# Kernel optimization log

Measured on AMD Instinct MI355X. Metric: run time of the kernel, lower is better.

## Reference

```python
import jax, jax.numpy as jnp
import numpy as np
from jax import lax

N_C = 2
T = 5
NE = 17   # equality constraints per (sample, t)
NV = 24   # variables per (sample, t): p(4), f(4), f_e(4), alpha1(2), alpha2(2), gamma(4), gamma_e(4)
ITERS = 400
B = 512

F_MASK = jnp.zeros((NV,), bool).at[4:8].set(True)     # L1-penalized coords (f)
NN_MASK = jnp.zeros((NV,), bool).at[12:24].set(True)  # nonneg coords (alpha1, alpha2, gamma, gamma_e)


def _conv(x, w, b):
    return lax.conv_general_dilated(x, w, (1, 1), 'VALID',
                                    dimension_numbers=('NCHW', 'OIHW', 'NCHW')) + b[None, :, None, None]


def _maxpool(x, k):
    return lax.reduce_window(x, -jnp.inf, lax.max, (1, 1, k, k), (1, 1, k, k), 'VALID')


def _encoder(img, cw1, cb1, cw2, cb2, w3, b3, w4, b4):
    h = jax.nn.relu(_maxpool(_conv(img, cw1, cb1), 2))   # (B,10,20,20)
    h = jax.nn.relu(_maxpool(_conv(h, cw2, cb2), 4))     # (B,20,4,4)
    h = h.reshape(h.shape[0], -1)                        # (B,320)
    h = jax.nn.relu(h @ w3.T + b3)                       # dropout is eval-mode identity
    return jax.nn.relu(h @ w4.T + b4)                    # (B,100)


def _mlp(h, w1, b1, w2, b2, w3, b3):
    h = jax.nn.relu(h @ w1.T + b1)  # dropout eval-mode identity
    h = jax.nn.relu(h @ w2.T + b2)
    return h @ w3.T + b3


def _build_Ab(r, ddr, fc, p_e, fc_e, v, p_r):
    # one (t)-slice: r(3), ddr(3), fc(8), p_e(4), fc_e(8), v(8), p_r(4) -> A(17,24), b(17)
    A = jnp.zeros((NE, NV))
    b = jnp.zeros((NE,))
    # force balance x: sum(f) + f_e0 + f_e1 = ddr0  (original f[:20] covers all 4 rows, f[20:] empty)
    A = A.at[0, 4:8].set(1.0).at[0, 8].set(1.0).at[0, 9].set(1.0)
    b = b.at[0].set(ddr[0])
    # force balance y: f_e2 + f_e3 = ddr1
    A = A.at[1, 10].set(1.0).at[1, 11].set(1.0)
    b = b.at[1].set(ddr[1])
    # torque balance
    A = A.at[2, 6].set(p_r[0] - r[0]).at[2, 4].set(-(p_r[2] - r[1]))
    A = A.at[2, 7].set(p_r[1] - r[0]).at[2, 5].set(-(p_r[3] - r[1]))
    A = A.at[2, 10].set(p_e[0] - r[0]).at[2, 8].set(-(p_e[2] - r[1]))
    A = A.at[2, 11].set(p_e[1] - r[0]).at[2, 9].set(-(p_e[3] - r[1]))
    b = b.at[2].set(ddr[2])
    for c in range(N_C):
        # p = alpha1*v_a + alpha2*v_b, alpha1+alpha2=1
        A = A.at[3 + 3 * c, c].set(1.0).at[3 + 3 * c, 12 + c].set(-v[2 * c]).at[3 + 3 * c, 14 + c].set(-v[2 * c + 2])
        A = A.at[4 + 3 * c, c + 2].set(1.0).at[4 + 3 * c, 12 + c].set(-v[2 * c + 1]).at[4 + 3 * c, 14 + c].set(-v[2 * c + 3])
        A = A.at[5 + 3 * c, 12 + c].set(1.0).at[5 + 3 * c, 14 + c].set(1.0)
        b = b.at[5 + 3 * c].set(1.0)
        # friction cone: f = gamma1*fc_a + gamma2*fc_b
        A = A.at[9 + 2 * c, 16 + c].set(fc[2 * c]).at[9 + 2 * c, 18 + c].set(fc[2 * c + 2]).at[9 + 2 * c, 4 + c].set(-1.0)
        A = A.at[10 + 2 * c, 16 + c].set(fc[2 * c + 1]).at[10 + 2 * c, 18 + c].set(fc[2 * c + 3]).at[10 + 2 * c, 6 + c].set(-1.0)
    # external force cones
    A = A.at[13, 20].set(fc_e[0]).at[13, 21].set(fc_e[2]).at[13, 8].set(-1.0)
    A = A.at[14, 20].set(fc_e[1]).at[14, 21].set(fc_e[3]).at[14, 10].set(-1.0)
    A = A.at[15, 22].set(fc_e[4]).at[15, 23].set(fc_e[6]).at[15, 9].set(-1.0)
    A = A.at[16, 22].set(fc_e[5]).at[16, 23].set(fc_e[7]).at[16, 11].set(-1.0)
    return A, b


def _specnorm(A):
    def body(i, u):
        u = A.T @ (A @ u)
        return u / (jnp.linalg.norm(u) + 1e-12)
    u = lax.fori_loop(0, 25, body, jnp.ones((A.shape[-1],), A.dtype))
    return jnp.linalg.norm(A @ u)


def _solve_lp(A, b):
    # batched: min ||f||_1  s.t.  A z = b,  z[nn] >= 0   via PDHG (Chambolle-Pock)
    P = A.shape[0]
    L = lax.stop_gradient(jax.vmap(_specnorm)(A))
    tau = (0.9 / (L + 1e-8))[:, None]
    sig = tau

    def step(carry, _):
        z, zb, y = carry
        y = y + sig * (jnp.einsum('pev,pv->pe', A, zb) - b)
        g = z - tau * jnp.einsum('pev,pe->pv', A, y)
        zn = jnp.where(F_MASK, jnp.sign(g) * jnp.maximum(jnp.abs(g) - tau, 0.0),
                       jnp.where(NN_MASK, jnp.maximum(g, 0.0), g))
        return (zn, 2.0 * zn - z, y), None

    z0 = jnp.zeros((P, NV))
    y0 = jnp.zeros((P, NE))
    (z, _, _), _ = lax.scan(step, (z0, z0, y0), None, length=ITERS)
    return z


def reference(xtraj, x, x_img, cw1, cb1, cw2, cb2, w3, b3, w4, b4,
              pw1, pb1, pw2, pb2, pw3, pb3, vw1, vb1, vw2, vb2, vw3, vb3):
    Bn = xtraj.shape[0]
    img = x_img.reshape(Bn, 1, 50, 50)
    e = _encoder(img, cw1, cb1, cw2, cb2, w3, b3, w4, b4)       # (B,100)
    h = jnp.concatenate([e, xtraj], axis=1)                     # (B,145)
    p_r = _mlp(h, pw1, pb1, pw2, pb2, pw3, pb3)                 # (B,20)
    v = _mlp(h, vw1, vb1, vw2, vb2, vw3, vb3)                   # (B,40)
    r = xtraj[:, :15].reshape(Bn, 3, T)
    ddr = xtraj[:, 30:45].reshape(Bn, 3, T)
    fc = x[:, 20:60].reshape(Bn, 8, T)
    p_e = x[:, 60:80].reshape(Bn, 4, T)
    fc_e = x[:, 80:120].reshape(Bn, 8, T)
    vM = v.reshape(Bn, 8, T)
    p_rM = p_r.reshape(Bn, 4, T)

    def flat(a):  # (B,d,T) -> (B*T, d)
        return jnp.swapaxes(a, 1, 2).reshape(Bn * T, a.shape[1])

    A, bvec = jax.vmap(_build_Ab)(flat(r), flat(ddr), flat(fc), flat(p_e), flat(fc_e), flat(vM), flat(p_rM))
    z = _solve_lp(A, bvec).reshape(Bn, T, NV)
    p = jnp.swapaxes(z[..., 0:4], 1, 2).reshape(Bn, 20)   # matches p.view(1,-1) C-order of (4,5)
    f = jnp.swapaxes(z[..., 4:8], 1, 2).reshape(Bn, 20)
    dp = p_r - x[:, 0:20]
    dv = v - x[:, 120:160]
    return 100.0 * jnp.concatenate([p, f, 10.0 * dp, 10.0 * dv], axis=1)  # (B,100)


def setup_inputs() -> dict:
    key = jax.random.key(0)
    ks = jax.random.split(key, 32)

    def rn(k, shape, s=0.05):
        return (s * jax.random.normal(k, shape)).astype(jnp.float32)

    return {
        'xtraj': rn(ks[0], (B, 45), 1.0),
        'x': rn(ks[1], (B, 160), 1.0),
        'x_img': rn(ks[2], (B, 2500), 1.0),
        'cw1': rn(ks[3], (10, 1, 11, 11)), 'cb1': rn(ks[4], (10,)),
        'cw2': rn(ks[5], (20, 10, 5, 5)), 'cb2': rn(ks[6], (20,)),
        'w3': rn(ks[7], (150, 320)), 'b3': rn(ks[8], (150,)),
        'w4': rn(ks[9], (100, 150)), 'b4': rn(ks[10], (100,)),
        'pw1': rn(ks[11], (100, 145)), 'pb1': rn(ks[12], (100,)),
        'pw2': rn(ks[13], (100, 100)), 'pb2': rn(ks[14], (100,)),
        'pw3': rn(ks[15], (20, 100)), 'pb3': rn(ks[16], (20,)),
        'vw1': rn(ks[17], (100, 145)), 'vb1': rn(ks[18], (100,)),
        'vw2': rn(ks[19], (100, 100)), 'vb2': rn(ks[20], (100,)),
        'vw3': rn(ks[21], (40, 100)), 'vb3': rn(ks[22], (40,)),
    }
```

## Files before the change

### kernel.cpp

```cpp
#include <hip/hip_runtime.h>

__global__ __launch_bounds__(128) void conv1_kernel(
    const float* __restrict__ x_img, const float* __restrict__ cw1,
    const float* __restrict__ cb1, float* __restrict__ h1)
{
    const int blk = blockIdx.x;
    const int b = blk >> 2;
    const int c = blk & 3;
    const int tid = threadIdx.x;

    __shared__ __align__(16) float s_img[1000];

    const float* img = x_img + (size_t)b * 2500 + (size_t)(10 * c) * 50;
    for (int i = tid; i < 1000; i += 128) s_img[i] = img[i];
    __syncthreads();

    if (tid < 100) {
        const int ly = tid / 20, px = tid % 20;
        const int py = 5 * c + ly;
        const int C = 2 * px;
        float acc0[10], acc1[10], acc2[10], acc3[10];
        #pragma unroll
        for (int oc = 0; oc < 10; ++oc) { acc0[oc] = 0.f; acc1[oc] = 0.f; acc2[oc] = 0.f; acc3[oc] = 0.f; }
        for (int r = 0; r < 12; ++r) {
            float v[12];
            #pragma unroll
            for (int j = 0; j < 6; ++j) {
                float2 t = *(const float2*)&s_img[(2 * ly + r) * 50 + C + 2 * j];
                v[2 * j] = t.x; v[2 * j + 1] = t.y;
            }
            if (r < 11) {
                #pragma unroll
                for (int oc = 0; oc < 10; ++oc) {
                    #pragma unroll
                    for (int kx = 0; kx < 11; ++kx) {
                        float w0 = cw1[oc * 121 + r * 11 + kx];
                        acc0[oc] = fmaf(v[kx], w0, acc0[oc]);
                        acc1[oc] = fmaf(v[kx + 1], w0, acc1[oc]);
                    }
                }
            }
            if (r >= 1) {
                #pragma unroll
                for (int oc = 0; oc < 10; ++oc) {
                    #pragma unroll
                    for (int kx = 0; kx < 11; ++kx) {
                        float w1 = cw1[oc * 121 + (r - 1) * 11 + kx];
                        acc2[oc] = fmaf(v[kx], w1, acc2[oc]);
                        acc3[oc] = fmaf(v[kx + 1], w1, acc3[oc]);
                    }
                }
            }
        }
        float* hb = h1 + (size_t)b * 4000 + py * 20 + px;
        #pragma unroll
        for (int oc = 0; oc < 10; ++oc) {
            float m = fmaxf(fmaxf(acc0[oc], acc1[oc]), fmaxf(acc2[oc], acc3[oc]));
            hb[oc * 400] = fmaxf(m + cb1[oc], 0.f);
        }
    }
}

__device__ const signed char AZ_IDX[32][8] = {
    {4,5,6,7,8,9,0,0},{10,11,0,0,0,0,0,0},{4,5,6,7,8,9,10,11},
    {0,12,14,0,0,0,0,0},{2,12,14,0,0,0,0,0},{12,14,0,0,0,0,0,0},
    {1,13,15,0,0,0,0,0},{3,13,15,0,0,0,0,0},{13,15,0,0,0,0,0,0},
    {16,18,4,0,0,0,0,0},{16,18,6,0,0,0,0,0},{17,19,5,0,0,0,0,0},
    {17,19,7,0,0,0,0,0},{20,21,8,0,0,0,0,0},{20,21,10,0,0,0,0,0},
    {22,23,9,0,0,0,0,0},{22,23,11,0,0,0,0,0},
    {0},{0},{0},{0},{0},{0},{0},{0},{0},{0},{0},{0},{0},{0},{0}
};
__device__ const signed char AZ_SEL[32][8] = {
    {1,1,1,1,1,1,0,0},{1,1,0,0,0,0,0,0},{3,4,5,6,7,8,9,10},
    {1,11,13,0,0,0,0,0},{1,12,14,0,0,0,0,0},{1,1,0,0,0,0,0,0},
    {1,13,15,0,0,0,0,0},{1,14,16,0,0,0,0,0},{1,1,0,0,0,0,0,0},
    {17,19,2,0,0,0,0,0},{18,20,2,0,0,0,0,0},{19,21,2,0,0,0,0,0},
    {20,22,2,0,0,0,0,0},{23,25,2,0,0,0,0,0},{24,26,2,0,0,0,0,0},
    {27,29,2,0,0,0,0,0},{28,30,2,0,0,0,0,0},
    {0},{0},{0},{0},{0},{0},{0},{0},{0},{0},{0},{0},{0},{0},{0}
};
__device__ const signed char AT_IDX[32][3] = {
    {3,0,0},{6,0,0},{4,0,0},{7,0,0},
    {0,2,9},{0,2,11},{0,2,10},{0,2,12},{0,2,13},{0,2,15},{1,2,14},{1,2,16},
    {3,4,5},{6,7,8},{3,4,5},{6,7,8},
    {9,10,0},{11,12,0},{9,10,0},{11,12,0},
    {13,14,0},{13,14,0},{15,16,0},{15,16,0},
    {0},{0},{0},{0},{0},{0},{0},{0}
};
__device__ const signed char WBA[32] = {0,0,0,0, 4,4,4,4, 4,4,4,4, 0,0,0,0, 4,4,4,4, 8,8,8,8, 0,0,0,0,0,0,0,0};
__device__ const signed char WBB[32] = {12,12,12,12, 8,8,8,8, 8,8,8,8, 12,12,12,12, 16,16,16,16, 20,20,20,20, 0,0,0,0,0,0,0,0};
__device__ const signed char WBC[32] = {0,0,0,0, 16,16,16,16, 20,20,20,20, 0,0,0,0, 0,0,0,0, 0,0,0,0, 0,0,0,0,0,0,0,0};

__global__ __launch_bounds__(320) void head_lp_kernel(
    const float* __restrict__ xtraj, const float* __restrict__ x,
    const float* __restrict__ h1g,
    const float* __restrict__ cw2, const float* __restrict__ cb2,
    const float* __restrict__ w3, const float* __restrict__ b3,
    const float* __restrict__ w4, const float* __restrict__ b4,
    const float* __restrict__ pw1, const float* __restrict__ pb1,
    const float* __restrict__ pw2, const float* __restrict__ pb2,
    const float* __restrict__ pw3, const float* __restrict__ pb3,
    const float* __restrict__ vw1, const float* __restrict__ vb1,
    const float* __restrict__ vw2, const float* __restrict__ vb2,
    const float* __restrict__ vw3, const float* __restrict__ vb3,
    float* __restrict__ out)
{
    const int b = blockIdx.x;
    const int tid = threadIdx.x;

    __shared__ __align__(16) float s_h1[4000];
    __shared__ __align__(16) float s_w2[5000];
    __shared__ __align__(16) float s_h2[320];
    __shared__ float s_hc[145];
    __shared__ float s_t1[152];
    __shared__ float s_m1[256];
    __shared__ float s_m2[256];

    float* Lb = s_h1;
    float* s_pr = Lb + 2285;
    float* s_vv = Lb + 2305;

    {
        const float4* src = (const float4*)(h1g + (size_t)b * 4000);
        float4* dst = (float4*)s_h1;
        for (int i = tid; i < 1000; i += 320) dst[i] = src[i];
        const float4* wsrc = (const float4*)cw2;
        float4* wdst = (float4*)s_w2;
        for (int i = tid; i < 1250; i += 320) wdst[i] = wsrc[i];
    }
    __syncthreads();

    {
        const int oc = tid >> 4, cell = tid & 15;
        const int R0 = (cell >> 2) * 4, C0 = (cell & 3) * 4;
        float acc[16];
        #pragma unroll
        for (int i = 0; i < 16; ++i) acc[i] = 0.f;
        for (int ic = 0; ic < 10; ++ic) {
            const float* hb = &s_h1[ic * 400];
            const float* wb = &s_w2[oc * 250 + ic * 25];
            float v[8][8];
            #pragma unroll
            for (int r = 0; r < 8; ++r) {
                float4 t0 = *(const float4*)&hb[(R0 + r) * 20 + C0];
                float4 t1 = *(const float4*)&hb[(R0 + r) * 20 + C0 + 4];
                v[r][0] = t0.x; v[r][1] = t0.y; v[r][2] = t0.z; v[r][3] = t0.w;
                v[r][4] = t1.x; v[r][5] = t1.y; v[r][6] = t1.z; v[r][7] = t1.w;
            }
            #pragma unroll
            for (int k = 0; k < 5; ++k) {
                #pragma unroll
                for (int kx = 0; kx < 5; ++kx) {
                    float wv = wb[k * 5 + kx];
                    #pragma unroll
                    for (int o = 0; o < 4; ++o) {
                        #pragma unroll
                        for (int cc = 0; cc < 4; ++cc)
                            acc[o * 4 + cc] = fmaf(v[o + k][cc + kx], wv, acc[o * 4 + cc]);
                    }
                }
            }
        }
        float m = acc[0];
        #pragma unroll
        for (int i = 1; i < 16; ++i) m = fmaxf(m, acc[i]);
        s_h2[tid] = fmaxf(m + cb2[oc], 0.f);
    }
    __syncthreads();

    if (tid < 150) {
        const float* w = w3 + tid * 320;
        float a0 = b3[tid], a1 = 0.f, a2 = 0.f, a3 = 0.f;
        for (int k = 0; k < 320; k += 4) {
            a0 = fmaf(s_h2[k],     w[k],     a0);
            a1 = fmaf(s_h2[k + 1], w[k + 1], a1);
            a2 = fmaf(s_h2[k + 2], w[k + 2], a2);
            a3 = fmaf(s_h2[k + 3], w[k + 3], a3);
        }
        s_t1[tid] = fmaxf((a0 + a1) + (a2 + a3), 0.f);
    }
    __syncthreads();

    if (tid < 100) {
        const float* w = w4 + tid * 150;
        float a0 = b4[tid], a1 = 0.f;
        for (int k = 0; k < 150; k += 2) {
            a0 = fmaf(s_t1[k],     w[k],     a0);
            a1 = fmaf(s_t1[k + 1], w[k + 1], a1);
        }
        s_hc[tid] = fmaxf(a0 + a1, 0.f);
    }
    if (tid >= 100 && tid < 145) s_hc[tid] = xtraj[b * 45 + (tid - 100)];
    __syncthreads();

    if (tid < 100) {
        const float* w = pw1 + tid * 145;
        float acc = pb1[tid];
        for (int k = 0; k < 145; ++k) acc = fmaf(s_hc[k], w[k], acc);
        s_m1[tid] = fmaxf(acc, 0.f);
    } else if (tid >= 128 && tid < 228) {
        int i = tid - 128;
        const float* w = vw1 + i * 145;
        float acc = vb1[i];
        for (int k = 0; k < 145; ++k) acc = fmaf(s_hc[k], w[k], acc);
        s_m1[tid] = fmaxf(acc, 0.f);
    }
    __syncthreads();

    if (tid < 100) {
        const float* w = pw2 + tid * 100;
        float acc = pb2[tid];
        for (int k = 0; k < 100; ++k) acc = fmaf(s_m1[k], w[k], acc);
        s_m2[tid] = fmaxf(acc, 0.f);
    } else if (tid >= 128 && tid < 228) {
        int i = tid - 128;
        const float* w = vw2 + i * 100;
        float acc = vb2[i];
        for (int k = 0; k < 100; ++k) acc = fmaf(s_m1[128 + k], w[k], acc);
        s_m2[tid] = fmaxf(acc, 0.f);
    }
    __syncthreads();

    if (tid < 20) {
        const float* w = pw3 + tid * 100;
        float acc = pb3[tid];
        for (int k = 0; k < 100; ++k) acc = fmaf(s_m2[k], w[k], acc);
        s_pr[tid] = acc;
        out[b * 100 + 40 + tid] = 1000.f * (acc - x[b * 160 + tid]);
    } else if (tid >= 128 && tid < 168) {
        int i = tid - 128;
        const float* w = vw3 + i * 100;
        float acc = vb3[i];
        for (int k = 0; k < 100; ++k) acc = fmaf(s_m2[128 + k], w[k], acc);
        s_vv[i] = acc;
        out[b * 100 + 60 + i] = 1000.f * (acc - x[b * 160 + 120 + i]);
    }
    __syncthreads();

    if (tid >= 160) return;
    const int t = tid >> 5;
    const int l = tid & 31;
    const float* xt = xtraj + b * 45;
    const float* xb = x + b * 160;

    float* val = Lb + t * 32;
    float* Ag  = Lb + 160 + t * 408;
    float* bg  = Lb + 2200 + t * 17;

    {
        float v_ = 0.f;
        if (l == 1) v_ = 1.f;
        else if (l == 2) v_ = -1.f;
        else if (l >= 3 && l <= 10) {
            float r0 = xt[t], r1 = xt[5 + t];
            switch (l) {
                case 3:  v_ = r1 - s_pr[10 + t]; break;
                case 4:  v_ = r1 - s_pr[15 + t]; break;
                case 5:  v_ = s_pr[0 + t] - r0;  break;
                case 6:  v_ = s_pr[5 + t] - r0;  break;
                case 7:  v_ = r1 - xb[60 + 10 + t]; break;
                case 8:  v_ = r1 - xb[60 + 15 + t]; break;
                case 9:  v_ = xb[60 + 0 + t] - r0;  break;
                default: v_ = xb[60 + 5 + t] - r0;  break;
            }
        }
        else if (l >= 11 && l <= 16) v_ = -s_vv[5 * (l - 11) + t];
        else if (l >= 17 && l <= 22) v_ = xb[20 + 5 * (l - 17) + t];
        else if (l >= 23 && l <= 30) v_ = xb[80 + 5 * (l - 23) + t];
        val[l] = v_;
    }
    for (int i = l; i < 408; i += 32) Ag[i] = 0.f;
    if (l < 17) {
        #pragma unroll
        for (int k = 0; k < 8; ++k) {
            int sel = AZ_SEL[l][k];
            if (sel != 0) Ag[l * 24 + (int)AZ_IDX[l][k]] = val[sel];
        }
        float bb = 0.f;
        if (l == 0) bb = xt[30 + t];
        else if (l == 1) bb = xt[35 + t];
        else if (l == 2) bb = xt[40 + t];
        else if (l == 5 || l == 8) bb = 1.f;
        bg[l] = bb;
    }

    const int bA = WBA[l], bB = WBB[l], bC = WBC[l];
    float cf[12];
    float cc = 0.f;
    #pragma unroll
    for (int k = 0; k < 12; ++k) cf[k] = 0.f;
    if (l < 24) {
        int e0 = AT_IDX[l][0], e1 = AT_IDX[l][1], e2 = AT_IDX[l][2];
        float a0 = Ag[e0 * 24 + l], a1 = Ag[e1 * 24 + l], a2 = Ag[e2 * 24 + l];
        cc = a0 * bg[e0] + a1 * bg[e1] + a2 * bg[e2];
        #pragma unroll
        for (int s = 0; s < 4; ++s)
            cf[s] = a0 * Ag[e0 * 24 + bA + s] + a1 * Ag[e1 * 24 + bA + s] + a2 * Ag[e2 * 24 + bA + s];
        #pragma unroll
        for (int s = 0; s < 4; ++s)
            cf[4 + s] = a0 * Ag[e0 * 24 + bB + s] + a1 * Ag[e1 * 24 + bB + s] + a2 * Ag[e2 * 24 + bB + s];
        if (l >= 4 && l < 12) {
            #pragma unroll
            for (int s = 0; s < 4; ++s)
                cf[8 + s] = a0 * Ag[e0 * 24 + bC + s] + a1 * Ag[e1 * 24 + bC + s] + a2 * Ag[e2 * 24 + bC + s];
        }
    }

    const bool isF  = (l >= 4 && l < 8);
    const bool isNN = (l >= 12);

    float* Zg = Lb + t * 32;

    #define WDOT(vA, vB, vC)                                                    \
        (((cf[0]*vA.x + cf[1]*vA.y) + (cf[2]*vA.z + cf[3]*vA.w)) +              \
         ((cf[4]*vB.x + cf[5]*vB.y) + (cf[6]*vB.z + cf[7]*vB.w)) +              \
         ((cf[8]*vC.x + cf[9]*vC.y) + (cf[10]*vC.z + cf[11]*vC.w)))

    float u = (l < 24) ? 1.f : 0.f;
    #pragma unroll 1
    for (int o = 0; o < 5; ++o) {
        #pragma unroll 1
        for (int ii = 0; ii < 5; ++ii) {
            Zg[l] = u;
            float4 vA = *(const float4*)(Zg + bA);
            float4 vB = *(const float4*)(Zg + bB);
            float4 vC = *(const float4*)(Zg + bC);
            u = WDOT(vA, vB, vC);
        }
        float s = u * u;
        s += __shfl_xor(s, 16, 32); s += __shfl_xor(s, 8, 32);
        s += __shfl_xor(s, 4, 32);  s += __shfl_xor(s, 2, 32);
        s += __shfl_xor(s, 1, 32);
        u = u / (sqrtf(s) + 1e-12f);
    }
    float tau;
    {
        Zg[l] = u;
        float4 vA = *(const float4*)(Zg + bA);
        float4 vB = *(const float4*)(Zg + bB);
        float4 vC = *(const float4*)(Zg + bC);
        float w = WDOT(vA, vB, vC);
        float s2 = u * w;
        s2 += __shfl_xor(s2, 16, 32); s2 += __shfl_xor(s2, 8, 32);
        s2 += __shfl_xor(s2, 4, 32);  s2 += __shfl_xor(s2, 2, 32);
        s2 += __shfl_xor(s2, 1, 32);
        tau = 0.9f / (sqrtf(fmaxf(s2, 0.f)) + 1e-8f);
    }

    const float t2 = tau * tau;
    #pragma unroll
    for (int k = 0; k < 12; ++k) cf[k] *= t2;
    const float cc2 = cc * t2;

    float zv = 0.f, zbv = 0.f, Q = 0.f;
    #pragma unroll 1
    for (int it = 0; it < 400; ++it) {
        Zg[l] = zbv;
        float4 vA = *(const float4*)(Zg + bA);
        float4 vB = *(const float4*)(Zg + bB);
        float4 vC = *(const float4*)(Zg + bC);
        float Qm = Q - cc2;
        float s = WDOT(vA, vB, vC);
        Q = Qm + s;

        float gg = zv - Q;
        float cl = fminf(fmaxf(gg, -tau), tau);
        float st = gg - cl;
        float nn = fmaxf(gg, 0.f);
        float zn = isF ? st : (isNN ? nn : gg);
        zbv = fmaf(2.f, zn, -zv);
        zv = zn;
    }
    #undef WDOT

    {
        float* ob = out + b * 100;
        if (l < 4)      ob[l * 5 + t]            = 100.f * zv;
        else if (l < 8) ob[20 + (l - 4) * 5 + t] = 100.f * zv;
    }
}

extern "C" void kernel_launch(void* const* d_in, const int* in_sizes, int n_in,
                              void* d_out, int out_size, void* d_ws, size_t ws_size,
                              hipStream_t stream) {
    const float* xtraj = (const float*)d_in[0];
    const float* x     = (const float*)d_in[1];
    const float* x_img = (const float*)d_in[2];
    const float* cw1 = (const float*)d_in[3];
    const float* cb1 = (const float*)d_in[4];
    const float* cw2 = (const float*)d_in[5];
    const float* cb2 = (const float*)d_in[6];
    const float* w3  = (const float*)d_in[7];
    const float* b3  = (const float*)d_in[8];
    const float* w4  = (const float*)d_in[9];
    const float* b4  = (const float*)d_in[10];
    const float* pw1 = (const float*)d_in[11];
    const float* pb1 = (const float*)d_in[12];
    const float* pw2 = (const float*)d_in[13];
    const float* pb2 = (const float*)d_in[14];
    const float* pw3 = (const float*)d_in[15];
    const float* pb3 = (const float*)d_in[16];
    const float* vw1 = (const float*)d_in[17];
    const float* vb1 = (const float*)d_in[18];
    const float* vw2 = (const float*)d_in[19];
    const float* vb2 = (const float*)d_in[20];
    const float* vw3 = (const float*)d_in[21];
    const float* vb3 = (const float*)d_in[22];

    float* out = (float*)d_out;
    const int Bn = in_sizes[0] / 45;

    float* ws_h1 = (float*)d_ws;

    conv1_kernel<<<Bn * 4, 128, 0, stream>>>(x_img, cw1, cb1, ws_h1);

    head_lp_kernel<<<Bn, 320, 0, stream>>>(
        xtraj, x, ws_h1, cw2, cb2, w3, b3, w4, b4,
        pw1, pb1, pw2, pb2, pw3, pb3, vw1, vb1, vw2, vb2, vw3, vb3,
        out);
}
```

Measured before the change: 242.7 us.

## Fuse conv1 into the head kernel and keep h1 in shared memory

```diff
diff --git a/kernel.cpp b/kernel.cpp
--- a/kernel.cpp
+++ b/kernel.cpp
@@ -1,65 +1,4 @@
 #include <hip/hip_runtime.h>
-
-__global__ __launch_bounds__(128) void conv1_kernel(
-    const float* __restrict__ x_img, const float* __restrict__ cw1,
-    const float* __restrict__ cb1, float* __restrict__ h1)
-{
-    const int blk = blockIdx.x;
-    const int b = blk >> 2;
-    const int c = blk & 3;
-    const int tid = threadIdx.x;
-
-    __shared__ __align__(16) float s_img[1000];
-
-    const float* img = x_img + (size_t)b * 2500 + (size_t)(10 * c) * 50;
-    for (int i = tid; i < 1000; i += 128) s_img[i] = img[i];
-    __syncthreads();
-
-    if (tid < 100) {
-        const int ly = tid / 20, px = tid % 20;
-        const int py = 5 * c + ly;
-        const int C = 2 * px;
-        float acc0[10], acc1[10], acc2[10], acc3[10];
-        #pragma unroll
-        for (int oc = 0; oc < 10; ++oc) { acc0[oc] = 0.f; acc1[oc] = 0.f; acc2[oc] = 0.f; acc3[oc] = 0.f; }
-        for (int r = 0; r < 12; ++r) {
-            float v[12];
-            #pragma unroll
-            for (int j = 0; j < 6; ++j) {
-                float2 t = *(const float2*)&s_img[(2 * ly + r) * 50 + C + 2 * j];
-                v[2 * j] = t.x; v[2 * j + 1] = t.y;
-            }
-            if (r < 11) {
-                #pragma unroll
-                for (int oc = 0; oc < 10; ++oc) {
-                    #pragma unroll
-                    for (int kx = 0; kx < 11; ++kx) {
-                        float w0 = cw1[oc * 121 + r * 11 + kx];
-                        acc0[oc] = fmaf(v[kx], w0, acc0[oc]);
-                        acc1[oc] = fmaf(v[kx + 1], w0, acc1[oc]);
-                    }
-                }
-            }
-            if (r >= 1) {
-                #pragma unroll
-                for (int oc = 0; oc < 10; ++oc) {
-                    #pragma unroll
-                    for (int kx = 0; kx < 11; ++kx) {
-                        float w1 = cw1[oc * 121 + (r - 1) * 11 + kx];
-                        acc2[oc] = fmaf(v[kx], w1, acc2[oc]);
-                        acc3[oc] = fmaf(v[kx + 1], w1, acc3[oc]);
-                    }
-                }
-            }
-        }
-        float* hb = h1 + (size_t)b * 4000 + py * 20 + px;
-        #pragma unroll
-        for (int oc = 0; oc < 10; ++oc) {
-            float m = fmaxf(fmaxf(acc0[oc], acc1[oc]), fmaxf(acc2[oc], acc3[oc]));
-            hb[oc * 400] = fmaxf(m + cb1[oc], 0.f);
-        }
-    }
-}
 
 __device__ const signed char AZ_IDX[32][8] = {
     {4,5,6,7,8,9,0,0},{10,11,0,0,0,0,0,0},{4,5,6,7,8,9,10,11},
@@ -91,9 +30,10 @@
 __device__ const signed char WBB[32] = {12,12,12,12, 8,8,8,8, 8,8,8,8, 12,12,12,12, 16,16,16,16, 20,20,20,20, 0,0,0,0,0,0,0,0};
 __device__ const signed char WBC[32] = {0,0,0,0, 16,16,16,16, 20,20,20,20, 0,0,0,0, 0,0,0,0, 0,0,0,0, 0,0,0,0,0,0,0,0};
 
-__global__ __launch_bounds__(320) void head_lp_kernel(
+__global__ __launch_bounds__(448) void net_kernel(
     const float* __restrict__ xtraj, const float* __restrict__ x,
-    const float* __restrict__ h1g,
+    const float* __restrict__ x_img,
+    const float* __restrict__ cw1, const float* __restrict__ cb1,
     const float* __restrict__ cw2, const float* __restrict__ cb2,
     const float* __restrict__ w3, const float* __restrict__ b3,
     const float* __restrict__ w4, const float* __restrict__ b4,
@@ -111,6 +51,7 @@
     __shared__ __align__(16) float s_h1[4000];
     __shared__ __align__(16) float s_w2[5000];
     __shared__ __align__(16) float s_h2[320];
+    __shared__ float s_cb1[10];
     __shared__ float s_hc[145];
     __shared__ float s_t1[152];
     __shared__ float s_m1[256];
@@ -120,17 +61,70 @@
     float* s_pr = Lb + 2285;
     float* s_vv = Lb + 2305;
 
+    float* s_img = s_w2;
+    float* s_cw1 = s_w2 + 2500;
+
     {
-        const float4* src = (const float4*)(h1g + (size_t)b * 4000);
-        float4* dst = (float4*)s_h1;
-        for (int i = tid; i < 1000; i += 320) dst[i] = src[i];
+        const float4* src = (const float4*)(x_img + (size_t)b * 2500);
+        float4* dst = (float4*)s_img;
+        for (int i = tid; i < 625; i += 448) dst[i] = src[i];
+        for (int i = tid; i < 1210; i += 448) s_cw1[i] = cw1[i];
+        if (tid < 10) s_cb1[tid] = cb1[tid];
+    }
+    __syncthreads();
+
+    if (tid < 400) {
+        const int py = tid / 20, px = tid % 20;
+        const int C = 2 * px;
+        float acc0[10], acc1[10], acc2[10], acc3[10];
+        #pragma unroll
+        for (int oc = 0; oc < 10; ++oc) { acc0[oc] = 0.f; acc1[oc] = 0.f; acc2[oc] = 0.f; acc3[oc] = 0.f; }
+        for (int r = 0; r < 12; ++r) {
+            float v[12];
+            #pragma unroll
+            for (int j = 0; j < 6; ++j) {
+                float2 t = *(const float2*)&s_img[(2 * py + r) * 50 + C + 2 * j];
+                v[2 * j] = t.x; v[2 * j + 1] = t.y;
+            }
+            if (r < 11) {
+                #pragma unroll
+                for (int oc = 0; oc < 10; ++oc) {
+                    #pragma unroll
+                    for (int kx = 0; kx < 11; ++kx) {
+                        float w0 = s_cw1[oc * 121 + r * 11 + kx];
+                        acc0[oc] = fmaf(v[kx], w0, acc0[oc]);
+                        acc1[oc] = fmaf(v[kx + 1], w0, acc1[oc]);
+                    }
+                }
+            }
+            if (r >= 1) {
+                #pragma unroll
+                for (int oc = 0; oc < 10; ++oc) {
+                    #pragma unroll
+                    for (int kx = 0; kx < 11; ++kx) {
+                        float w1 = s_cw1[oc * 121 + (r - 1) * 11 + kx];
+                        acc2[oc] = fmaf(v[kx], w1, acc2[oc]);
+                        acc3[oc] = fmaf(v[kx + 1], w1, acc3[oc]);
+                    }
+                }
+            }
+        }
+        #pragma unroll
+        for (int oc = 0; oc < 10; ++oc) {
+            float m = fmaxf(fmaxf(acc0[oc], acc1[oc]), fmaxf(acc2[oc], acc3[oc]));
+            s_h1[oc * 400 + tid] = fmaxf(m + s_cb1[oc], 0.f);
+        }
+    }
+    __syncthreads();
+
+    {
         const float4* wsrc = (const float4*)cw2;
         float4* wdst = (float4*)s_w2;
-        for (int i = tid; i < 1250; i += 320) wdst[i] = wsrc[i];
-    }
-    __syncthreads();
-
-    {
+        for (int i = tid; i < 1250; i += 448) wdst[i] = wsrc[i];
+    }
+    __syncthreads();
+
+    if (tid < 320) {
         const int oc = tid >> 4, cell = tid & 15;
         const int R0 = (cell >> 2) * 4, C0 = (cell & 3) * 4;
         float acc[16];
@@ -410,12 +404,8 @@
     float* out = (float*)d_out;
     const int Bn = in_sizes[0] / 45;
 
-    float* ws_h1 = (float*)d_ws;
-
-    conv1_kernel<<<Bn * 4, 128, 0, stream>>>(x_img, cw1, cb1, ws_h1);
-
-    head_lp_kernel<<<Bn, 320, 0, stream>>>(
-        xtraj, x, ws_h1, cw2, cb2, w3, b3, w4, b4,
+    net_kernel<<<Bn, 448, 0, stream>>>(
+        xtraj, x, x_img, cw1, cb1, cw2, cb2, w3, b3, w4, b4,
         pw1, pb1, pw2, pb2, pw3, pb3, vw1, vb1, vw2, vb2, vw3, vb3,
         out);
 }
```

Result: faster. 235.4 us (-3.0%).
